# Performance work log

Measured on AMD Instinct MI355X. Metric: run time of the kernel, lower is better.

## Reference

```python
import jax, jax.numpy as jnp
import numpy as np

D_MODEL = 1024
N_HEADS = 16
D_FF = 4096
WINDOW = 256
EPS = 1e-5


def setup_inputs() -> dict:
    key = jax.random.key(0)
    ks = jax.random.split(key, 12)
    B, T, C = 4, 1024, D_MODEL
    s = lambda fan: 1.0 / np.sqrt(fan)
    return {
        "x": jax.random.normal(ks[0], (B, T, C), jnp.float32),
        "Wqkv": jax.random.normal(ks[1], (3 * C, C), jnp.float32) * s(C),
        "bqkv": jnp.zeros((3 * C,), jnp.float32),
        "Wo": jax.random.normal(ks[2], (C, C), jnp.float32) * s(C),
        "bo": jnp.zeros((C,), jnp.float32),
        "W1": jax.random.normal(ks[3], (D_FF, C), jnp.float32) * s(C),
        "b1": jnp.zeros((D_FF,), jnp.float32),
        "W2": jax.random.normal(ks[4], (C, D_FF), jnp.float32) * s(D_FF),
        "b2": jnp.zeros((C,), jnp.float32),
        "g1": jnp.ones((C,), jnp.float32),
        "be1": jnp.zeros((C,), jnp.float32),
        "g2": jnp.ones((C,), jnp.float32),
        "be2": jnp.zeros((C,), jnp.float32),
    }


def _layernorm(x, g, b):
    mu = jnp.mean(x, axis=-1, keepdims=True)
    var = jnp.mean(jnp.square(x - mu), axis=-1, keepdims=True)
    return (x - mu) * jax.lax.rsqrt(var + EPS) * g + b


def reference(x, Wqkv, bqkv, Wo, bo, W1, b1, W2, b2, g1, be1, g2, be2):
    B, T, C = x.shape
    H, Dh = N_HEADS, C // N_HEADS
    # QKV projection (torch MultiheadAttention packed in_proj)
    qkv = jnp.einsum("btc,ec->bte", x, Wqkv) + bqkv  # [B,T,3C]
    q, k, v = jnp.split(qkv, 3, axis=-1)
    q = q.reshape(B, T, H, Dh).transpose(0, 2, 1, 3)  # [B,H,T,Dh]
    k = k.reshape(B, T, H, Dh).transpose(0, 2, 1, 3)
    v = v.reshape(B, T, H, Dh).transpose(0, 2, 1, 3)
    scores = jnp.einsum("bhqd,bhkd->bhqk", q, k) / jnp.sqrt(jnp.float32(Dh))
    # causal banded mask: key j visible to query i iff 0 <= i-j < WINDOW
    i = jnp.arange(T)[:, None]
    j = jnp.arange(T)[None, :]
    band = (j <= i) & (i - j < WINDOW)
    scores = jnp.where(band, scores, -jnp.inf)
    attn = jax.nn.softmax(scores, axis=-1)
    ctx = jnp.einsum("bhqk,bhkd->bhqd", attn, v)  # [B,H,T,Dh]
    ctx = ctx.transpose(0, 2, 1, 3).reshape(B, T, C)
    attn_out = jnp.einsum("btc,oc->bto", ctx, Wo) + bo
    x = _layernorm(x + attn_out, g1, be1)
    h = jax.nn.gelu(jnp.einsum("btc,fc->btf", x, W1) + b1, approximate=False)
    ffn_out = jnp.einsum("btf,cf->btc", h, W2) + b2
    return _layernorm(x + ffn_out, g2, be2)
```

## Files before the change

### kernel.cpp

```cpp
#include <hip/hip_runtime.h>
#include <hip/hip_bf16.h>

typedef __attribute__((ext_vector_type(4))) float floatx4;
typedef __attribute__((ext_vector_type(8))) short shortx8;

struct bf4 { __hip_bfloat16 h[4]; };
union U8 { shortx8 v; __hip_bfloat16 h[8]; };
union U4 { unsigned long long v; __hip_bfloat16 h[4]; };

__device__ __forceinline__ void async_copy16(const __hip_bfloat16* g, __hip_bfloat16* l) {
  __builtin_amdgcn_global_load_lds((__attribute__((address_space(1))) void*)g,
                                   (__attribute__((address_space(3))) void*)l,
                                   16, 0, 0);
}

__global__ __launch_bounds__(256) void cast_all_kernel(
    const float* __restrict__ s0, __hip_bfloat16* __restrict__ d0, int nb0,
    const float* __restrict__ s1, __hip_bfloat16* __restrict__ d1, int nb1,
    const float* __restrict__ s2, __hip_bfloat16* __restrict__ d2, int nb2,
    const float* __restrict__ s3, __hip_bfloat16* __restrict__ d3, int nb3,
    const float* __restrict__ s4, __hip_bfloat16* __restrict__ d4) {
  int b = blockIdx.x;
  const float* src; __hip_bfloat16* dst;
  if (b < nb0) { src = s0; dst = d0; }
  else { b -= nb0;
    if (b < nb1) { src = s1; dst = d1; }
    else { b -= nb1;
      if (b < nb2) { src = s2; dst = d2; }
      else { b -= nb2;
        if (b < nb3) { src = s3; dst = d3; }
        else { b -= nb3; src = s4; dst = d4; }
      }
    }
  }
  const int i = b * 256 + threadIdx.x;
  const float4 v = ((const float4*)src)[i];
  bf4 o4;
  o4.h[0] = __float2bfloat16(v.x);
  o4.h[1] = __float2bfloat16(v.y);
  o4.h[2] = __float2bfloat16(v.z);
  o4.h[3] = __float2bfloat16(v.w);
  *(bf4*)(dst + (size_t)i * 4) = o4;
}

#define STG_A(slot, kt, ks)                                                    \
  async_copy16(Ag + (size_t)(kt) * 64 + (size_t)(ks) * 32,                     \
               &As[slot][tid * 8]);                                            \
  async_copy16(Ag + (size_t)128 * K + (size_t)(kt) * 64 + (size_t)(ks) * 32,   \
               &As[slot][4096 + tid * 8]);

#define STG_B(slot, kt, ks)                                                    \
  async_copy16(Bg + (size_t)(kt) * 64 + (size_t)(ks) * 32,                     \
               &Bs[slot][tid * 8]);                                            \
  async_copy16(Bg + (size_t)128 * K + (size_t)(kt) * 64 + (size_t)(ks) * 32,   \
               &Bs[slot][4096 + tid * 8]);

#define G256_PHASE(SLOT, MH, BLOAD, STAGE_CODE, WAIT_CODE)                     \
  {                                                                            \
    const __hip_bfloat16* Asl = As[SLOT];                                      \
    const __hip_bfloat16* Bsl = Bs[SLOT];                                      \
    if (BLOAD) {                                                               \
      _Pragma("unroll")                                                        \
      for (int ni = 0; ni < 4; ++ni)                                           \
        bfr[ni] = *(const shortx8*)&Bsl[brd + ni * 512];                       \
    }                                                                          \
    shortx8 afr[4];                                                            \
    _Pragma("unroll")                                                          \
    for (int mi4 = 0; mi4 < 4; ++mi4)                                          \
      afr[mi4] = *(const shortx8*)&Asl[ard + ((MH) * 4 + mi4) * 512];          \
    STAGE_CODE;                                                                \
    WAIT_CODE;                                                                 \
    __builtin_amdgcn_s_barrier();                                              \
    asm volatile("s_waitcnt lgkmcnt(0)" ::: "memory");                         \
    __builtin_amdgcn_sched_barrier(0);                                         \
    __builtin_amdgcn_s_setprio(1);                                             \
    _Pragma("unroll")                                                          \
    for (int mi4 = 0; mi4 < 4; ++mi4)                                          \
      _Pragma("unroll")                                                        \
      for (int ni = 0; ni < 4; ++ni)                                           \
        acc[(MH) * 4 + mi4][ni] = __builtin_amdgcn_mfma_f32_16x16x32_bf16(     \
            afr[mi4], bfr[ni], acc[(MH) * 4 + mi4][ni], 0, 0, 0);              \
    __builtin_amdgcn_s_setprio(0);                                             \
    __builtin_amdgcn_s_barrier();                                              \
  }

#define G256_KLOOP()                                                           \
  STG_A(0, 0, 0) STG_B(0, 0, 0)                                                \
  STG_A(1, 0, 1) STG_B(1, 0, 1)                                                \
  STG_A(2, 1, 0) STG_B(2, 1, 0)                                                \
  asm volatile("s_waitcnt vmcnt(8)" ::: "memory");                             \
  __builtin_amdgcn_s_barrier();                                                \
  shortx8 bfr[4];                                                              \
  for (int T = 0; T < NKT; ++T) {                                              \
    const int s00 = (2 * T) & 3;                                               \
    const int s01 = (2 * T + 1) & 3;                                           \
    const int sn1 = (2 * T + 3) & 3;                           \
    const int sn0 = (2 * T + 4) & 3;                           \
    const bool st1 = (T + 1 < NKT);                                            \
    const bool st2 = (T + 2 < NKT);                                            \
    G256_PHASE(s00, 0, true,                                                   \
               { if (st1) { STG_A(sn1, T + 1, 1) } },                          \
               {})                                                             \
    G256_PHASE(s00, 1, false,                                                  \
               { if (st1) { STG_B(sn1, T + 1, 1) } },                          \
               { if (st1) { asm volatile("s_waitcnt vmcnt(8)" ::: "memory"); } \
                 else     { asm volatile("s_waitcnt vmcnt(0)" ::: "memory"); } })\
    G256_PHASE(s01, 0, true,                                                   \
               { if (st2) { STG_A(sn0, T + 2, 0) } },                          \
               {})                                                             \
    G256_PHASE(s01, 1, false,                                                  \
               { if (st2) { STG_B(sn0, T + 2, 0) } },                          \
               { if (st2)      { asm volatile("s_waitcnt vmcnt(8)" ::: "memory"); }\
                 else if (st1) { asm volatile("s_waitcnt vmcnt(4)" ::: "memory"); } })\
  }

template<int EPI>
__global__ __launch_bounds__(512, 2) void gemm256(
    const __hip_bfloat16* __restrict__ A,
    const __hip_bfloat16* __restrict__ B,
    const float* __restrict__ bias,
    __hip_bfloat16* __restrict__ outb,
    int M, int N, int K, int NT)
{
  __shared__ __align__(16) __hip_bfloat16 As[4][256 * 32];
  __shared__ __align__(16) __hip_bfloat16 Bs[4][256 * 32];
  const int tid  = threadIdx.x;
  const int lane = tid & 63;
  const int wave = tid >> 6;
  const int wr = wave >> 2;
  const int wc = wave & 3;
  const int fr = lane & 15;
  const int fq = lane >> 4;

  const int nwg = gridDim.x;
  const int cpx = nwg >> 3;
  const int swz = (blockIdx.x & 7) * cpx + (blockIdx.x >> 3);
  const int mt = swz / NT, nt = swz % NT;
  const long bm = (long)mt * 256, bn = (long)nt * 256;

  const int srow = tid >> 2;
  const int sch  = (tid & 3) ^ ((tid >> 3) & 3);
  const __hip_bfloat16* Ag = A + (bm + srow) * (size_t)K + sch * 8;
  const __hip_bfloat16* Bg = B + (bn + srow) * (size_t)K + sch * 8;

  const int swc = (fq ^ ((fr >> 1) & 3)) << 3;
  const int ard = (wr * 128 + fr) * 32 + swc;
  const int brd = (wc * 64 + fr) * 32 + swc;

  const floatx4 zero = {0.f, 0.f, 0.f, 0.f};
  floatx4 acc[8][4];
#pragma unroll
  for (int mi = 0; mi < 8; ++mi)
#pragma unroll
    for (int ni = 0; ni < 4; ++ni) acc[mi][ni] = zero;

  const int NKT = K >> 6;
  G256_KLOOP()

#pragma unroll
  for (int mi = 0; mi < 8; ++mi) {
#pragma unroll
    for (int ni = 0; ni < 4; ++ni) {
      const long col = bn + wc * 64 + ni * 16 + fr;
      const float bv = bias[col];
#pragma unroll
      for (int r = 0; r < 4; ++r) {
        const long row = bm + wr * 128 + mi * 16 + fq * 4 + r;
        float v = acc[mi][ni][r] + bv;
        if (EPI == 1) {
          const float u = v + 0.044715f * v * v * v;
          v = v / (1.0f + __expf(-1.5957691216057308f * u));
        }
        outb[(size_t)row * N + col] = __float2bfloat16(v);
      }
    }
  }
}

__global__ __launch_bounds__(512, 2) void gemm256_splitk(
    const __hip_bfloat16* __restrict__ A,
    const __hip_bfloat16* __restrict__ B,
    __hip_bfloat16* __restrict__ part,
    int M, int N, int K, int Klen, int NT, int TPS)
{
  __shared__ __align__(16) __hip_bfloat16 As[4][256 * 32];
  __shared__ __align__(16) __hip_bfloat16 Bs[4][256 * 32];
  const int tid  = threadIdx.x;
  const int lane = tid & 63;
  const int wave = tid >> 6;
  const int wr = wave >> 2;
  const int wc = wave & 3;
  const int fr = lane & 15;
  const int fq = lane >> 4;

  const int nwg = gridDim.x;
  const int cpx = nwg >> 3;
  const int swz = (blockIdx.x & 7) * cpx + (blockIdx.x >> 3);
  const int zt = swz / TPS;
  const int tile = swz % TPS;
  const int mt = tile / NT, nt = tile % NT;
  const long bm = (long)mt * 256, bn = (long)nt * 256;
  const int kstart = zt * Klen;

  const int srow = tid >> 2;
  const int sch  = (tid & 3) ^ ((tid >> 3) & 3);
  const __hip_bfloat16* Ag = A + (bm + srow) * (size_t)K + kstart + sch * 8;
  const __hip_bfloat16* Bg = B + (bn + srow) * (size_t)K + kstart + sch * 8;

  const int swc = (fq ^ ((fr >> 1) & 3)) << 3;
  const int ard = (wr * 128 + fr) * 32 + swc;
  const int brd = (wc * 64 + fr) * 32 + swc;

  const floatx4 zero = {0.f, 0.f, 0.f, 0.f};
  floatx4 acc[8][4];
#pragma unroll
  for (int mi = 0; mi < 8; ++mi)
#pragma unroll
    for (int ni = 0; ni < 4; ++ni) acc[mi][ni] = zero;

  const int NKT = Klen >> 6;
  G256_KLOOP()

  __hip_bfloat16* outp = part + (size_t)zt * M * N;
#pragma unroll
  for (int mi = 0; mi < 8; ++mi) {
#pragma unroll
    for (int ni = 0; ni < 4; ++ni) {
      const long col = bn + wc * 64 + ni * 16 + fr;
#pragma unroll
      for (int r = 0; r < 4; ++r) {
        const long row = bm + wr * 128 + mi * 16 + fq * 4 + r;
        outp[(size_t)row * N + col] = __float2bfloat16(acc[mi][ni][r]);
      }
    }
  }
}

#define GEMM_SWIZZLE()                                                        \
  const int flat = blockIdx.x + gridDim.x * (blockIdx.y + 32 * blockIdx.z);   \
  const int xcd_ = flat & 7;                                                  \
  int rsw_ = flat >> 3;                                                       \
  const int mt_ = xcd_ * 4 + (rsw_ & 3);                                      \
  rsw_ >>= 2;                                                                 \
  const int nt_ = rsw_ % gridDim.x;                                           \
  const int zt_ = rsw_ / gridDim.x;

#define GEMM_STAGE(buf, koff)                                      \
  async_copy16(Ag0 + (koff),           &Asl[buf][tid * 8]);        \
  async_copy16(Ag0 + (koff) + rstride, &Asl[buf][tid * 8 + 2048]); \
  async_copy16(Bg0 + (koff),           &Bsl[buf][tid * 8]);        \
  async_copy16(Bg0 + (koff) + rstride, &Bsl[buf][tid * 8 + 2048]);

#define GEMM_KLOOP(NI)                                                        \
  GEMM_STAGE(0, 0)                                                            \
  GEMM_STAGE(1, 32)                                                           \
  int cur = 0;                                                                \
  for (int it = 0; it < (NI); ++it) {                                         \
    if (it + 2 < (NI)) {                                                      \
      const int nb = (cur >= 1) ? cur - 1 : cur + 2;           \
      GEMM_STAGE(nb, (it + 2) * 32)                                           \
      asm volatile("s_waitcnt vmcnt(8)" ::: "memory");                        \
    } else if (it + 1 < (NI)) {                                               \
      asm volatile("s_waitcnt vmcnt(4)" ::: "memory");                        \
    } else {                                                                  \
      asm volatile("s_waitcnt vmcnt(0)" ::: "memory");                        \
    }                                                                         \
    asm volatile("s_barrier" ::: "memory");                                   \
    const __hip_bfloat16* Ac = Asl[cur];                                      \
    const __hip_bfloat16* Bc = Bsl[cur];                                      \
    shortx8 afr[4], bfr[4];                                                   \
    _Pragma("unroll")                                                         \
    for (int i = 0; i < 4; ++i) {                                             \
      afr[i] = *(const shortx8*)&Ac[(wr * 64 + i * 16 + fr) * 32 + sw];       \
      bfr[i] = *(const shortx8*)&Bc[(wc * 64 + i * 16 + fr) * 32 + sw];       \
    }                                                                         \
    _Pragma("unroll")                                                         \
    for (int mi = 0; mi < 4; ++mi)                                            \
      _Pragma("unroll")                                                       \
      for (int ni = 0; ni < 4; ++ni)                                          \
        acc[mi][ni] = __builtin_amdgcn_mfma_f32_16x16x32_bf16(                \
            afr[mi], bfr[ni], acc[mi][ni], 0, 0, 0);                          \
    asm volatile("s_barrier" ::: "memory");                                   \
    cur = (cur == 2) ? 0 : cur + 1;                                           \
  }

__global__ __launch_bounds__(256) void gemm_bt_splitk(
    const __hip_bfloat16* __restrict__ A,
    const __hip_bfloat16* __restrict__ B,
    __hip_bfloat16* __restrict__ part,
    int M, int N, int K, int Klen)
{
  __shared__ __align__(16) __hip_bfloat16 Asl[3][128 * 32];
  __shared__ __align__(16) __hip_bfloat16 Bsl[3][128 * 32];
  const int tid  = threadIdx.x;
  const int lane = tid & 63;
  const int wave = tid >> 6;
  const int wr = wave >> 1, wc = wave & 1;
  GEMM_SWIZZLE()
  const long bm = (long)mt_ * 128, bn = (long)nt_ * 128;
  const int kstart = zt_ * Klen;

  const int srow = tid >> 2;
  const int scol = ((((tid & 3) - (tid >> 3)) & 3) << 3);
  const __hip_bfloat16* Ag0 = A + (bm + srow) * (long)K + kstart + scol;
  const __hip_bfloat16* Bg0 = B + (bn + srow) * (long)K + kstart + scol;
  const long rstride = 64l * K;

  const int fr = lane & 15;
  const int fq = lane >> 4;
  const int sw = (((fq + ((fr >> 1) & 3)) & 3) << 3);

  const floatx4 zero = {0.f, 0.f, 0.f, 0.f};
  floatx4 acc[4][4];
#pragma unroll
  for (int mi = 0; mi < 4; ++mi)
#pragma unroll
    for (int ni = 0; ni < 4; ++ni) acc[mi][ni] = zero;

  const int NI = Klen >> 5;
  GEMM_KLOOP(NI)

  __hip_bfloat16* outp = part + (size_t)zt_ * M * N;
#pragma unroll
  for (int mi = 0; mi < 4; ++mi) {
#pragma unroll
    for (int ni = 0; ni < 4; ++ni) {
      const long col = bn + wc * 64 + ni * 16 + fr;
#pragma unroll
      for (int r = 0; r < 4; ++r) {
        const long row = bm + wr * 64 + mi * 16 + fq * 4 + r;
        outp[(size_t)row * N + col] = __float2bfloat16(acc[mi][ni][r]);
      }
    }
  }
}

__global__ __launch_bounds__(256) void transpose_v_kernel(
    const __hip_bfloat16* __restrict__ qkv, __hip_bfloat16* __restrict__ vt)
{
  const int bh = blockIdx.y;
  const int tt = blockIdx.x;
  const int b = bh >> 4, h = bh & 15;
  __shared__ __hip_bfloat16 tile[64][65];
  const int tid = threadIdx.x;
  const int r = tid >> 2;
  const int c = (tid & 3) << 4;
  const __hip_bfloat16* src = qkv + (size_t)(b * 1024 + tt * 64 + r) * 3072 + 2048 + h * 64 + c;
  U8 u0, u1;
  u0.v = *(const shortx8*)src;
  u1.v = *(const shortx8*)(src + 8);
#pragma unroll
  for (int j = 0; j < 8; ++j) { tile[r][c + j] = u0.h[j]; tile[r][c + 8 + j] = u1.h[j]; }
  __syncthreads();
  U8 w0, w1;
#pragma unroll
  for (int j = 0; j < 8; ++j) { w0.h[j] = tile[c + j][r]; w1.h[j] = tile[c + 8 + j][r]; }
  __hip_bfloat16* dst = vt + ((size_t)bh * 64 + r) * 1024 + tt * 64 + c;
  *(shortx8*)dst       = w0.v;
  *(shortx8*)(dst + 8) = w1.v;
}

__global__ __launch_bounds__(256) void attn_kernel(
    const __hip_bfloat16* __restrict__ qkv,
    const __hip_bfloat16* __restrict__ vt,
    __hip_bfloat16* __restrict__ ctx)
{
  const int wave = threadIdx.x >> 6;
  const int lane = threadIdx.x & 63;
  const int gw = blockIdx.x * 4 + wave;
  const int qt = gw & 63;
  const int bh = gw >> 6;
  const int b = bh >> 4, h = bh & 15;
  const int fr = lane & 15, fq = lane >> 4;
  const int q0 = qt << 4;

  __shared__ __align__(16) __hip_bfloat16 Plds[4][16 * 32];
  __hip_bfloat16* Pw = Plds[wave];

  const __hip_bfloat16* qrow = qkv + (size_t)(b * 1024 + q0 + fr) * 3072 + h * 64;
  const shortx8 aq0 = *(const shortx8*)(qrow + fq * 8);
  const shortx8 aq1 = *(const shortx8*)(qrow + 32 + fq * 8);

  const float SC = 0.125f * 1.44269504088896f;
  float m_r[4] = {-1e30f, -1e30f, -1e30f, -1e30f};
  float l_r[4] = {0.f, 0.f, 0.f, 0.f};
  const floatx4 zero = {0.f, 0.f, 0.f, 0.f};
  floatx4 o[4];
#pragma unroll
  for (int nd = 0; nd < 4; ++nd) o[nd] = zero;

  const int kt0 = (q0 >= 255) ? ((q0 - 255) >> 5) : 0;
  const int kt1 = (q0 + 15) >> 5;
  for (int kt = kt0; kt <= kt1; ++kt) {
    const int kbase = kt << 5;
    const __hip_bfloat16* krow0 = qkv + (size_t)(b * 1024 + kbase + fr) * 3072 + 1024 + h * 64;
    const __hip_bfloat16* krow1 = krow0 + 16 * 3072;
    const shortx8 bk00 = *(const shortx8*)(krow0 + fq * 8);
    const shortx8 bk01 = *(const shortx8*)(krow0 + 32 + fq * 8);
    const shortx8 bk10 = *(const shortx8*)(krow1 + fq * 8);
    const shortx8 bk11 = *(const shortx8*)(krow1 + 32 + fq * 8);
    floatx4 s0 = zero, s1 = zero;
    s0 = __builtin_amdgcn_mfma_f32_16x16x32_bf16(aq0, bk00, s0, 0, 0, 0);
    s0 = __builtin_amdgcn_mfma_f32_16x16x32_bf16(aq1, bk01, s0, 0, 0, 0);
    s1 = __builtin_amdgcn_mfma_f32_16x16x32_bf16(aq0, bk10, s1, 0, 0, 0);
    s1 = __builtin_amdgcn_mfma_f32_16x16x32_bf16(aq1, bk11, s1, 0, 0, 0);
#pragma unroll
    for (int r = 0; r < 4; ++r) { s0[r] *= SC; s1[r] *= SC; }
    if (kbase + 31 > q0 || kbase < q0 - 240) {
#pragma unroll
      for (int r = 0; r < 4; ++r) {
        const int tq = q0 + fq * 4 + r;
        const int j0 = kbase + fr;
        const int j1 = j0 + 16;
        if (j0 > tq || j0 < tq - 255) s0[r] = -3e38f;
        if (j1 > tq || j1 < tq - 255) s1[r] = -3e38f;
      }
    }
#pragma unroll
    for (int r = 0; r < 4; ++r) {
      float vmax = fmaxf(s0[r], s1[r]);
      vmax = fmaxf(vmax, __shfl_xor(vmax, 1));
      vmax = fmaxf(vmax, __shfl_xor(vmax, 2));
      vmax = fmaxf(vmax, __shfl_xor(vmax, 4));
      vmax = fmaxf(vmax, __shfl_xor(vmax, 8));
      const float mnew = fmaxf(m_r[r], vmax);
      const float alpha = exp2f(m_r[r] - mnew);
      const float p0 = exp2f(s0[r] - mnew);
      const float p1 = exp2f(s1[r] - mnew);
      m_r[r] = mnew;
      float ps = p0 + p1;
      ps += __shfl_xor(ps, 1);
      ps += __shfl_xor(ps, 2);
      ps += __shfl_xor(ps, 4);
      ps += __shfl_xor(ps, 8);
      l_r[r] = l_r[r] * alpha + ps;
      o[0][r] *= alpha; o[1][r] *= alpha; o[2][r] *= alpha; o[3][r] *= alpha;
      Pw[(fq * 4 + r) * 32 + fr]      = __float2bfloat16(p0);
      Pw[(fq * 4 + r) * 32 + 16 + fr] = __float2bfloat16(p1);
    }
    asm volatile("s_waitcnt lgkmcnt(0)" ::: "memory");
    const shortx8 ap = *(const shortx8*)&Pw[fr * 32 + fq * 8];
#pragma unroll
    for (int nd = 0; nd < 4; ++nd) {
      const shortx8 bv = *(const shortx8*)&vt[((size_t)bh * 64 + nd * 16 + fr) * 1024 + kbase + fq * 8];
      o[nd] = __builtin_amdgcn_mfma_f32_16x16x32_bf16(ap, bv, o[nd], 0, 0, 0);
    }
    asm volatile("s_waitcnt lgkmcnt(0)" ::: "memory");
  }
#pragma unroll
  for (int nd = 0; nd < 4; ++nd)
#pragma unroll
    for (int r = 0; r < 4; ++r)
      ctx[(size_t)(b * 1024 + q0 + fq * 4 + r) * 1024 + h * 64 + nd * 16 + fr] =
          __float2bfloat16(o[nd][r] / l_r[r]);
}

template<int S, int WB>
__global__ __launch_bounds__(256) void ln_sum_kernel(
    const __hip_bfloat16* __restrict__ part,
    const float* __restrict__ resid,
    const float* __restrict__ bias,
    const float* __restrict__ g, const float* __restrict__ be,
    float* __restrict__ outf, __hip_bfloat16* __restrict__ outb)
{
  const int row = blockIdx.x;
  const int tid = threadIdx.x;
  const size_t base = (size_t)row * 1024;
  float4 v = ((const float4*)(resid + base))[tid];
  const float4 bv = ((const float4*)bias)[tid];
  v.x += bv.x; v.y += bv.y; v.z += bv.z; v.w += bv.w;
#pragma unroll
  for (int s = 0; s < S; ++s) {
    U4 p;
    p.v = *(const unsigned long long*)&part[(size_t)s * 4096 * 1024 + base + tid * 4];
    v.x += __bfloat162float(p.h[0]);
    v.y += __bfloat162float(p.h[1]);
    v.z += __bfloat162float(p.h[2]);
    v.w += __bfloat162float(p.h[3]);
  }
  float sm = v.x + v.y + v.z + v.w;
  float ss = v.x * v.x + v.y * v.y + v.z * v.z + v.w * v.w;
#pragma unroll
  for (int off = 1; off < 64; off <<= 1) {
    sm += __shfl_xor(sm, off);
    ss += __shfl_xor(ss, off);
  }
  __shared__ float red[8];
  if ((tid & 63) == 0) { red[tid >> 6] = sm; red[4 + (tid >> 6)] = ss; }
  __syncthreads();
  sm = red[0] + red[1] + red[2] + red[3];
  ss = red[4] + red[5] + red[6] + red[7];
  const float mu = sm * (1.0f / 1024.0f);
  const float rs = rsqrtf(ss * (1.0f / 1024.0f) - mu * mu + 1e-5f);
  const float4 gg = ((const float4*)g)[tid];
  const float4 bb = ((const float4*)be)[tid];
  float4 y;
  y.x = (v.x - mu) * rs * gg.x + bb.x;
  y.y = (v.y - mu) * rs * gg.y + bb.y;
  y.z = (v.z - mu) * rs * gg.z + bb.z;
  y.w = (v.w - mu) * rs * gg.w + bb.w;
  ((float4*)(outf + base))[tid] = y;
  if (WB) {
    bf4 o4;
    o4.h[0] = __float2bfloat16(y.x);
    o4.h[1] = __float2bfloat16(y.y);
    o4.h[2] = __float2bfloat16(y.z);
    o4.h[3] = __float2bfloat16(y.w);
    *(bf4*)(outb + base + tid * 4) = o4;
  }
}

extern "C" void kernel_launch(void* const* d_in, const int* in_sizes, int n_in,
                              void* d_out, int out_size, void* d_ws, size_t ws_size,
                              hipStream_t stream) {
  const float* x    = (const float*)d_in[0];
  const float* Wqkv = (const float*)d_in[1];
  const float* bqkv = (const float*)d_in[2];
  const float* Wo   = (const float*)d_in[3];
  const float* bo   = (const float*)d_in[4];
  const float* W1   = (const float*)d_in[5];
  const float* b1   = (const float*)d_in[6];
  const float* W2   = (const float*)d_in[7];
  const float* b2   = (const float*)d_in[8];
  const float* g1   = (const float*)d_in[9];
  const float* be1  = (const float*)d_in[10];
  const float* g2   = (const float*)d_in[11];
  const float* be2  = (const float*)d_in[12];

  char* ws = (char*)d_ws;
  size_t off = 0;
  auto alloc = [&](size_t bytes) -> void* {
    void* p = ws + off;
    off += (bytes + 255) & ~(size_t)255;
    return p;
  };
  __hip_bfloat16* wqkvb = (__hip_bfloat16*)alloc(6291456);
  __hip_bfloat16* wob   = (__hip_bfloat16*)alloc(2097152);
  __hip_bfloat16* w1b   = (__hip_bfloat16*)alloc(8388608);
  __hip_bfloat16* w2b   = (__hip_bfloat16*)alloc(8388608);
  __hip_bfloat16* xb    = (__hip_bfloat16*)alloc(8388608);
  __hip_bfloat16* qkvb  = (__hip_bfloat16*)alloc(25165824);
  __hip_bfloat16* vtb   = (__hip_bfloat16*)alloc(8388608);
  __hip_bfloat16* ctxb  = (__hip_bfloat16*)alloc(8388608);
  __hip_bfloat16* part  = (__hip_bfloat16*)alloc(4u * 8388608);
  float*          x1f   = (float*)alloc(16777216);
  __hip_bfloat16* x1b   = (__hip_bfloat16*)alloc(8388608);
  __hip_bfloat16* hb    = (__hip_bfloat16*)alloc(33554432);
  (void)ws_size; (void)in_sizes; (void)n_in; (void)out_size;

  cast_all_kernel<<<16384, 256, 0, stream>>>(x, xb, 4096,
                                             Wqkv, wqkvb, 3072,
                                             Wo, wob, 1024,
                                             W1, w1b, 4096,
                                             W2, w2b);
  gemm256<0><<<192, 512, 0, stream>>>(xb, wqkvb, bqkv, qkvb, 4096, 3072, 1024, 12);
  transpose_v_kernel<<<dim3(16, 64), 256, 0, stream>>>(qkvb, vtb);
  attn_kernel<<<1024, 256, 0, stream>>>(qkvb, vtb, ctxb);
  gemm_bt_splitk<<<dim3(8, 32, 2), 256, 0, stream>>>(ctxb, wob, part, 4096, 1024, 1024, 512);
  ln_sum_kernel<2, 1><<<4096, 256, 0, stream>>>(part, x, bo, g1, be1, x1f, x1b);
  gemm256<1><<<256, 512, 0, stream>>>(x1b, w1b, b1, hb, 4096, 4096, 1024, 16);
  gemm256_splitk<<<256, 512, 0, stream>>>(hb, w2b, part, 4096, 1024, 4096, 1024, 4, 64);
  ln_sum_kernel<4, 0><<<4096, 256, 0, stream>>>(part, x1f, b2, g2, be2, (float*)d_out, nullptr);
}
```

Before: 326.6 us.

## Software-pipeline LDS fragment reads one phase ahead of MFMAs in gemm256 K-loop

Restructures the gemm256 K-loop so the A/B fragments for the next phase are read from LDS while the current phase's MFMAs run, using double fragment registers (a0/a1, bE/bO). It drops the per-phase lgkmcnt(0) wait and one of the two barriers per phase, and reorders vmcnt waits. This targets the LDS-read latency that sat before every MFMA block. In exchange it needs more VGPRs under launch_bounds(512,2), and the changed barrier and waitcnt ordering risks LDS races if the slot reuse is mis-sequenced.

```diff
diff --git a/kernel.cpp b/kernel.cpp
--- a/kernel.cpp
+++ b/kernel.cpp
@@ -55,63 +55,75 @@
   async_copy16(Bg + (size_t)128 * K + (size_t)(kt) * 64 + (size_t)(ks) * 32,   \
                &Bs[slot][4096 + tid * 8]);
 
-#define G256_PHASE(SLOT, MH, BLOAD, STAGE_CODE, WAIT_CODE)                     \
-  {                                                                            \
-    const __hip_bfloat16* Asl = As[SLOT];                                      \
-    const __hip_bfloat16* Bsl = Bs[SLOT];                                      \
-    if (BLOAD) {                                                               \
-      _Pragma("unroll")                                                        \
-      for (int ni = 0; ni < 4; ++ni)                                           \
-        bfr[ni] = *(const shortx8*)&Bsl[brd + ni * 512];                       \
-    }                                                                          \
-    shortx8 afr[4];                                                            \
+#define G256_READ_A(dst, slot, mh)                                             \
+  _Pragma("unroll")                                                            \
+  for (int i_ = 0; i_ < 4; ++i_)                                               \
+    dst[i_] = *(const shortx8*)&As[slot][ard + ((mh) * 4 + i_) * 512];
+
+#define G256_READ_B(dst, slot)                                                 \
+  _Pragma("unroll")                                                            \
+  for (int i_ = 0; i_ < 4; ++i_)                                               \
+    dst[i_] = *(const shortx8*)&Bs[slot][brd + i_ * 512];
+
+#define G256_MFMA(afr, bfr, MH)                                                \
+  __builtin_amdgcn_sched_barrier(0);                                           \
+  __builtin_amdgcn_s_setprio(1);                                               \
+  _Pragma("unroll")                                                            \
+  for (int mi_ = 0; mi_ < 4; ++mi_)                                            \
     _Pragma("unroll")                                                          \
-    for (int mi4 = 0; mi4 < 4; ++mi4)                                          \
-      afr[mi4] = *(const shortx8*)&Asl[ard + ((MH) * 4 + mi4) * 512];          \
-    STAGE_CODE;                                                                \
-    WAIT_CODE;                                                                 \
-    __builtin_amdgcn_s_barrier();                                              \
-    asm volatile("s_waitcnt lgkmcnt(0)" ::: "memory");                         \
-    __builtin_amdgcn_sched_barrier(0);                                         \
-    __builtin_amdgcn_s_setprio(1);                                             \
-    _Pragma("unroll")                                                          \
-    for (int mi4 = 0; mi4 < 4; ++mi4)                                          \
-      _Pragma("unroll")                                                        \
-      for (int ni = 0; ni < 4; ++ni)                                           \
-        acc[(MH) * 4 + mi4][ni] = __builtin_amdgcn_mfma_f32_16x16x32_bf16(     \
-            afr[mi4], bfr[ni], acc[(MH) * 4 + mi4][ni], 0, 0, 0);              \
-    __builtin_amdgcn_s_setprio(0);                                             \
-    __builtin_amdgcn_s_barrier();                                              \
-  }
+    for (int ni_ = 0; ni_ < 4; ++ni_)                                          \
+      acc[(MH) * 4 + mi_][ni_] = __builtin_amdgcn_mfma_f32_16x16x32_bf16(      \
+          afr[mi_], bfr[ni_], acc[(MH) * 4 + mi_][ni_], 0, 0, 0);              \
+  __builtin_amdgcn_s_setprio(0);                                               \
+  __builtin_amdgcn_sched_barrier(0);
+
+#define G256_BAR() asm volatile("s_barrier" ::: "memory")
 
 #define G256_KLOOP()                                                           \
   STG_A(0, 0, 0) STG_B(0, 0, 0)                                                \
   STG_A(1, 0, 1) STG_B(1, 0, 1)                                                \
   STG_A(2, 1, 0) STG_B(2, 1, 0)                                                \
   asm volatile("s_waitcnt vmcnt(8)" ::: "memory");                             \
-  __builtin_amdgcn_s_barrier();                                                \
-  shortx8 bfr[4];                                                              \
+  G256_BAR();                                                                  \
+  shortx8 a0[4], a1[4], bE[4], bO[4];                                          \
+  G256_READ_B(bE, 0)                                                           \
+  G256_READ_A(a0, 0, 0)                                                        \
   for (int T = 0; T < NKT; ++T) {                                              \
     const int s00 = (2 * T) & 3;                                               \
     const int s01 = (2 * T + 1) & 3;                                           \
+    const int sx  = (2 * T + 2) & 3;                           \
     const int sn1 = (2 * T + 3) & 3;                           \
     const int sn0 = (2 * T + 4) & 3;                           \
     const bool st1 = (T + 1 < NKT);                                            \
     const bool st2 = (T + 2 < NKT);                                            \
-    G256_PHASE(s00, 0, true,                                                   \
-               { if (st1) { STG_A(sn1, T + 1, 1) } },                          \
-               {})                                                             \
-    G256_PHASE(s00, 1, false,                                                  \
-               { if (st1) { STG_B(sn1, T + 1, 1) } },                          \
-               { if (st1) { asm volatile("s_waitcnt vmcnt(8)" ::: "memory"); } \
-                 else     { asm volatile("s_waitcnt vmcnt(0)" ::: "memory"); } })\
-    G256_PHASE(s01, 0, true,                                                   \
-               { if (st2) { STG_A(sn0, T + 2, 0) } },                          \
-               {})                                                             \
-    G256_PHASE(s01, 1, false,                                                  \
-               { if (st2) { STG_B(sn0, T + 2, 0) } },                          \
-               { if (st2)      { asm volatile("s_waitcnt vmcnt(8)" ::: "memory"); }\
-                 else if (st1) { asm volatile("s_waitcnt vmcnt(4)" ::: "memory"); } })\
+                                                                       \
+    G256_BAR();                                                                \
+    if (st1) { asm volatile("s_waitcnt vmcnt(4)" ::: "memory"); }              \
+    else     { asm volatile("s_waitcnt vmcnt(0)" ::: "memory"); }              \
+    G256_READ_A(a1, s00, 1)                                                    \
+    if (st1) { STG_A(sn1, T + 1, 1) }                                          \
+    G256_MFMA(a0, bE, 0)                                                       \
+                                                                       \
+    G256_BAR();                                                                \
+    G256_READ_B(bO, s01)                                                       \
+    G256_READ_A(a0, s01, 0)                                                    \
+    if (st1) { STG_B(sn1, T + 1, 1) }                                          \
+    G256_MFMA(a1, bE, 1)                                                       \
+                                                                       \
+    G256_BAR();                                                                \
+    if (st1) { asm volatile("s_waitcnt vmcnt(4)" ::: "memory"); }              \
+    else     { asm volatile("s_waitcnt vmcnt(0)" ::: "memory"); }              \
+    G256_READ_A(a1, s01, 1)                                                    \
+    if (st2) { STG_A(sn0, T + 2, 0) }                                          \
+    G256_MFMA(a0, bO, 0)                                                       \
+                                                                       \
+    G256_BAR();                                                                \
+    if (st1) {                                                                 \
+      G256_READ_B(bE, sx)                                                      \
+      G256_READ_A(a0, sx, 0)                                                   \
+    }                                                                          \
+    if (st2) { STG_B(sn0, T + 2, 0) }                                          \
+    G256_MFMA(a1, bO, 1)                                                       \
   }
 
 template<int EPI>
```

Result: no change. 321.2 us (-1.6%).
